# Optimization experiments

Measured on AMD Instinct MI355X. Metric: run time of the kernel, lower is better.

## Reference

```python
import jax, jax.numpy as jnp
import numpy as np

S, B, H = 4096, 32, 512

def setup_inputs() -> dict:
    key = jax.random.key(0)
    k1, k2, k3, k4, k5 = jax.random.split(key, 5)
    hidden = jax.random.normal(k1, (1, B, H), dtype=jnp.float32)
    encoder_outputs = jax.random.normal(k2, (S, B, H), dtype=jnp.float32)
    embedding = jax.random.normal(k3, (S, B, 3), dtype=jnp.float32)
    # learned params (xavier-ish scale)
    bigram_matrix = jax.random.normal(k4, (H, H), dtype=jnp.float32) * (1.0 / np.sqrt(H))
    affect_matrix = jax.random.normal(k5, (H, 3), dtype=jnp.float32) * 0.1
    return {"hidden": hidden, "encoder_outputs": encoder_outputs,
            "embedding": embedding, "bigram_matrix": bigram_matrix,
            "affect_matrix": affect_matrix}

def reference(hidden, encoder_outputs, embedding, bigram_matrix, affect_matrix):
    # hidden: [1,B,H] -> [B,H] (view(-1) over single layer)
    h = hidden[0]
    # bigram-modulated encoder states:
    #   i == 0: enc[0]
    #   i  > 0: (enc[i-1] @ W_bigram) * enc[i]
    modulated = jnp.einsum('sbh,hk->sbk', encoder_outputs[:-1], bigram_matrix) * encoder_outputs[1:]
    bigram_hidden = jnp.concatenate([encoder_outputs[:1], modulated], axis=0)  # [S,B,H]
    # dot-attention energy per (b, s)
    e_dot = jnp.einsum('sbh,bh->bs', bigram_hidden, h)  # [B,S]
    # affect term: (h @ affect_matrix) . embedding[s,b]
    e_aff = jnp.einsum('bk,sbk->bs', jnp.einsum('bh,hk->bk', h, affect_matrix), embedding)
    attn = jax.nn.softmax(e_dot + e_aff, axis=-1)  # softmax over seq dim
    return attn[:, None, :]  # [B,1,S]
```

## Files before the change

kernel.cpp:

```cpp
#include <hip/hip_runtime.h>
#include <cstdint>
#include <cstddef>

#define S_DIM 4096
#define B_DIM 32
#define H_DIM 512
#define M_DIM (S_DIM * B_DIM)

typedef unsigned short u16;
typedef unsigned int u32;
typedef float f32x4 __attribute__((ext_vector_type(4)));
typedef __bf16 bf16x8 __attribute__((ext_vector_type(8)));

__device__ __forceinline__ u16 f2bf(float v) {
    union { float f; u32 u; } a; a.f = v;
    u32 r = a.u + 0x7fffu + ((a.u >> 16) & 1u);
    return (u16)(r >> 16);
}
__device__ __forceinline__ float bf2f(u16 b) {
    union { float f; u32 u; } a; a.u = ((u32)b) << 16; return a.f;
}
__device__ __forceinline__ void split_bf(float v, u16& h, u16& l) {
    h = f2bf(v);
    l = f2bf(v - bf2f(h));
}

__device__ __forceinline__ void gl2lds16(const void* g, void* l) {
    __builtin_amdgcn_global_load_lds(
        (const __attribute__((address_space(1))) unsigned int*)g,
        (__attribute__((address_space(3))) unsigned int*)l,
        16, 0, 0);
}

__global__ void prep_w(const float* __restrict__ W,
                       u16* __restrict__ Wh, u16* __restrict__ Wl) {
    int i = blockIdx.x * 256 + threadIdx.x;
    float w = W[i];
    u16 h, l;
    split_bf(w, h, l);
    Wh[i] = h; Wl[i] = l;
}

__device__ __forceinline__ void split4_store(
    float4 e, float4 h, u16* dh, u16* dl)
{
    float vf[4] = { e.x * h.x, e.y * h.y, e.z * h.z, e.w * h.w };
    u32 rh[4], rl[4];
    #pragma unroll
    for (int i = 0; i < 4; ++i) {
        const u32 u = __float_as_uint(vf[i]);
        rh[i] = (u + 0x7fffu + ((u >> 16) & 1u)) & 0xffff0000u;
        const float lo_f = vf[i] - __uint_as_float(rh[i]);
        const u32 ul = __float_as_uint(lo_f);
        rl[i] = ul + 0x7fffu + ((ul >> 16) & 1u);
    }
    uint2 hw, lw;
    hw.x = rh[1] | (rh[0] >> 16);
    hw.y = rh[3] | (rh[2] >> 16);
    lw.x = (rl[1] & 0xffff0000u) | (rl[0] >> 16);
    lw.y = (rl[3] & 0xffff0000u) | (rl[2] >> 16);
    *(uint2*)dh = hw;
    *(uint2*)dl = lw;
}

__global__ __launch_bounds__(256, 2) void bigram_gemm_fused(
    const float* __restrict__ enc,
    const float* __restrict__ hid,
    const u16* __restrict__ Wh, const u16* __restrict__ Wl,
    float* __restrict__ Lp)
{
    __shared__ u16 sAh[2][128 * 32];
    __shared__ u16 sAl[2][128 * 32];
    __shared__ u16 sBh[2][128 * 32];
    __shared__ u16 sBl[2][128 * 32];
    __shared__ float rowsum[2][128];

    const int tid  = threadIdx.x;
    const int wave = tid >> 6;
    const int lane = tid & 63;
    const int wr   = wave >> 1;
    const int wc   = wave & 1;
    const int logical = (blockIdx.x & 7) * 512 + (blockIdx.x >> 3);
    const int jt   = logical & 3;
    const int mt   = logical >> 2;
    const int m0   = mt * 128;
    const int j0   = jt * 128;
    const int g    = lane >> 4;
    const int cl   = lane & 15;

    const int srow = wave * 32 + (lane >> 2);
    const int scol = (lane & 3) * 8;
    const size_t boff0 = (size_t)(j0 + srow) * H_DIM + scol;
    const size_t boff1 = boff0 + (size_t)16 * H_DIM;
    const u16* pBh0 = Wh + boff0; const u16* pBh1 = Wh + boff1;
    const u16* pBl0 = Wl + boff0; const u16* pBl1 = Wl + boff1;
    const int d0 = wave * 1024, d1 = d0 + 512;

    const int abrow = tid >> 3;
    const int akq   = tid & 7;
    const float* pe0 = enc + (size_t)(m0 +  0 + abrow) * H_DIM + akq * 4;
    const float* pe1 = enc + (size_t)(m0 + 32 + abrow) * H_DIM + akq * 4;
    const float* pe2 = enc + (size_t)(m0 + 64 + abrow) * H_DIM + akq * 4;
    const float* pe3 = enc + (size_t)(m0 + 96 + abrow) * H_DIM + akq * 4;
    const float* ph  = hid + (size_t)abrow * H_DIM + akq * 4;
    const int awoff = abrow * 32 + akq * 4;

    f32x4 acc[4][4];
    #pragma unroll
    for (int mf = 0; mf < 4; ++mf)
        #pragma unroll
        for (int nf = 0; nf < 4; ++nf)
            acc[mf][nf] = (f32x4){0.f, 0.f, 0.f, 0.f};

    {
        gl2lds16(pBh0, &sBh[0][d0]);
        gl2lds16(pBh1, &sBh[0][d1]);
        gl2lds16(pBl0, &sBl[0][d0]);
        gl2lds16(pBl1, &sBl[0][d1]);
        const float4 h0 = *(const float4*)ph;
        const float4 e0 = *(const float4*)pe0;
        const float4 e1 = *(const float4*)pe1;
        const float4 e2 = *(const float4*)pe2;
        const float4 e3 = *(const float4*)pe3;
        split4_store(e0, h0, &sAh[0][0 * 1024 + awoff], &sAl[0][0 * 1024 + awoff]);
        split4_store(e1, h0, &sAh[0][1 * 1024 + awoff], &sAl[0][1 * 1024 + awoff]);
        split4_store(e2, h0, &sAh[0][2 * 1024 + awoff], &sAl[0][2 * 1024 + awoff]);
        split4_store(e3, h0, &sAh[0][3 * 1024 + awoff], &sAl[0][3 * 1024 + awoff]);
    }
    __syncthreads();

    #pragma unroll 2
    for (int kt = 0; kt < 16; ++kt) {
        const int cur = kt & 1, nxt = cur ^ 1;
        const int ko = (kt + 1) * 32;

        float4 e0n, e1n, e2n, e3n, hn;
        if (kt < 15) {
            gl2lds16(pBh0 + ko, &sBh[nxt][d0]);
            gl2lds16(pBh1 + ko, &sBh[nxt][d1]);
            gl2lds16(pBl0 + ko, &sBl[nxt][d0]);
            gl2lds16(pBl1 + ko, &sBl[nxt][d1]);
            e0n = *(const float4*)(pe0 + ko);
            e1n = *(const float4*)(pe1 + ko);
            e2n = *(const float4*)(pe2 + ko);
            e3n = *(const float4*)(pe3 + ko);
            hn  = *(const float4*)(ph + ko);
        }

        bf16x8 ah[4], al[4], bh[4], bl[4];
        #pragma unroll
        for (int mf = 0; mf < 4; ++mf) {
            const int ar = wr * 64 + mf * 16 + cl;
            ah[mf] = *(const bf16x8*)(&sAh[cur][ar * 32 + g * 8]);
            al[mf] = *(const bf16x8*)(&sAl[cur][ar * 32 + g * 8]);
        }
        #pragma unroll
        for (int nf = 0; nf < 4; ++nf) {
            const int br = wc * 64 + nf * 16 + cl;
            bh[nf] = *(const bf16x8*)(&sBh[cur][br * 32 + g * 8]);
            bl[nf] = *(const bf16x8*)(&sBl[cur][br * 32 + g * 8]);
        }
        #pragma unroll
        for (int mf = 0; mf < 4; ++mf)
            #pragma unroll
            for (int nf = 0; nf < 4; ++nf) {
                acc[mf][nf] = __builtin_amdgcn_mfma_f32_16x16x32_bf16(ah[mf], bh[nf], acc[mf][nf], 0, 0, 0);
                acc[mf][nf] = __builtin_amdgcn_mfma_f32_16x16x32_bf16(ah[mf], bl[nf], acc[mf][nf], 0, 0, 0);
                acc[mf][nf] = __builtin_amdgcn_mfma_f32_16x16x32_bf16(al[mf], bh[nf], acc[mf][nf], 0, 0, 0);
            }

        if (kt < 15) {
            split4_store(e0n, hn, &sAh[nxt][0 * 1024 + awoff], &sAl[nxt][0 * 1024 + awoff]);
            split4_store(e1n, hn, &sAh[nxt][1 * 1024 + awoff], &sAl[nxt][1 * 1024 + awoff]);
            split4_store(e2n, hn, &sAh[nxt][2 * 1024 + awoff], &sAl[nxt][2 * 1024 + awoff]);
            split4_store(e3n, hn, &sAh[nxt][3 * 1024 + awoff], &sAl[nxt][3 * 1024 + awoff]);
        }
        __syncthreads();
    }

    #pragma unroll
    for (int mf = 0; mf < 4; ++mf) {
        float rs0 = 0.f, rs1 = 0.f, rs2 = 0.f, rs3 = 0.f;
        const int growb = m0 + wr * 64 + mf * 16 + g * 4;
        #pragma unroll
        for (int nf = 0; nf < 4; ++nf) {
            const int gcol = j0 + wc * 64 + nf * 16 + cl;
            float e0 = (growb + 0 >= B_DIM) ? enc[(size_t)(growb + 0 - B_DIM) * H_DIM + gcol] : 0.f;
            float e1 = (growb + 1 >= B_DIM) ? enc[(size_t)(growb + 1 - B_DIM) * H_DIM + gcol] : 0.f;
            float e2 = (growb + 2 >= B_DIM) ? enc[(size_t)(growb + 2 - B_DIM) * H_DIM + gcol] : 0.f;
            float e3 = (growb + 3 >= B_DIM) ? enc[(size_t)(growb + 3 - B_DIM) * H_DIM + gcol] : 0.f;
            rs0 += acc[mf][nf][0] * e0;
            rs1 += acc[mf][nf][1] * e1;
            rs2 += acc[mf][nf][2] * e2;
            rs3 += acc[mf][nf][3] * e3;
        }
        #pragma unroll
        for (int off = 1; off < 16; off <<= 1) {
            rs0 += __shfl_xor(rs0, off);
            rs1 += __shfl_xor(rs1, off);
            rs2 += __shfl_xor(rs2, off);
            rs3 += __shfl_xor(rs3, off);
        }
        if (cl == 0) {
            const int rb = wr * 64 + mf * 16 + g * 4;
            rowsum[wc][rb + 0] = rs0;
            rowsum[wc][rb + 1] = rs1;
            rowsum[wc][rb + 2] = rs2;
            rowsum[wc][rb + 3] = rs3;
        }
    }
    __syncthreads();
    if (tid < 128) {
        const int gm = m0 + tid;
        if (gm >= B_DIM) {
            Lp[(size_t)jt * M_DIM + (size_t)(gm & 31) * S_DIM + (gm >> 5)] =
                rowsum[0][tid] + rowsum[1][tid];
        }
    }
}

__global__ __launch_bounds__(256) void prep_aff(
    const float* __restrict__ enc,
    const float* __restrict__ hid,
    const float* __restrict__ aff,
    float* __restrict__ Aux)
{
    __shared__ float w[4][4];
    const int b    = blockIdx.x;
    const int tid  = threadIdx.x;
    const int wave = tid >> 6;
    const int lane = tid & 63;

    float p0 = 0.f, p1 = 0.f, p2 = 0.f, p3 = 0.f;
    #pragma unroll
    for (int it = 0; it < 2; ++it) {
        const int h = tid + it * 256;
        const float hv = hid[b * H_DIM + h];
        p0 += hv * aff[h * 3 + 0];
        p1 += hv * aff[h * 3 + 1];
        p2 += hv * aff[h * 3 + 2];
        p3 += hv * enc[(size_t)b * H_DIM + h];
    }
    #pragma unroll
    for (int off = 32; off > 0; off >>= 1) {
        p0 += __shfl_xor(p0, off);
        p1 += __shfl_xor(p1, off);
        p2 += __shfl_xor(p2, off);
        p3 += __shfl_xor(p3, off);
    }
    if (lane == 0) { w[wave][0] = p0; w[wave][1] = p1; w[wave][2] = p2; w[wave][3] = p3; }
    __syncthreads();
    if (tid < 4)
        Aux[b * 4 + tid] = w[0][tid] + w[1][tid] + w[2][tid] + w[3][tid];
}

__global__ __launch_bounds__(256) void sm_partial(
    const float* __restrict__ emb,
    const float* __restrict__ Lp,
    const float* __restrict__ Aux,
    float* __restrict__ Lg,
    float* __restrict__ Part)
{
    __shared__ float wm[4];
    __shared__ float wsum[4];
    const int b     = blockIdx.x >> 3;
    const int strip = blockIdx.x & 7;
    const int tid   = threadIdx.x;
    const int wave  = tid >> 6;
    const int lane  = tid & 63;

    const float ha0 = Aux[b * 4 + 0], ha1 = Aux[b * 4 + 1],
                ha2 = Aux[b * 4 + 2], s0dot = Aux[b * 4 + 3];

    float lgv[2];
    float mx = -3.4e38f;
    #pragma unroll
    for (int it = 0; it < 2; ++it) {
        const int s = strip * 512 + it * 256 + tid;
        const size_t base = (size_t)b * S_DIM + s;
        const float ed = (s == 0) ? s0dot
            : (Lp[base] + Lp[(size_t)M_DIM + base] + Lp[2 * (size_t)M_DIM + base] + Lp[3 * (size_t)M_DIM + base]);
        const float* e = emb + (size_t)(s * B_DIM + b) * 3;
        const float lg = ed + ha0 * e[0] + ha1 * e[1] + ha2 * e[2];
        Lg[(size_t)b * S_DIM + s] = lg;
        lgv[it] = lg;
        mx = fmaxf(mx, lg);
    }
    #pragma unroll
    for (int off = 32; off > 0; off >>= 1) mx = fmaxf(mx, __shfl_xor(mx, off));
    if (lane == 0) wm[wave] = mx;
    __syncthreads();
    mx = fmaxf(fmaxf(wm[0], wm[1]), fmaxf(wm[2], wm[3]));

    float sum = __expf(lgv[0] - mx) + __expf(lgv[1] - mx);
    #pragma unroll
    for (int off = 32; off > 0; off >>= 1) sum += __shfl_xor(sum, off);
    if (lane == 0) wsum[wave] = sum;
    __syncthreads();
    if (tid == 0) {
        Part[(size_t)(b * 8 + strip) * 2 + 0] = mx;
        Part[(size_t)(b * 8 + strip) * 2 + 1] = wsum[0] + wsum[1] + wsum[2] + wsum[3];
    }
}

__global__ __launch_bounds__(256) void sm_final(
    const float* __restrict__ Lg,
    const float* __restrict__ Part,
    float* __restrict__ out)
{
    const int b     = blockIdx.x >> 3;
    const int strip = blockIdx.x & 7;
    const int tid   = threadIdx.x;

    float M = -3.4e38f;
    #pragma unroll
    for (int i = 0; i < 8; ++i) M = fmaxf(M, Part[(size_t)(b * 8 + i) * 2]);
    float S = 0.f;
    #pragma unroll
    for (int i = 0; i < 8; ++i)
        S += Part[(size_t)(b * 8 + i) * 2 + 1] * __expf(Part[(size_t)(b * 8 + i) * 2] - M);
    const float inv = 1.0f / S;

    #pragma unroll
    for (int it = 0; it < 2; ++it) {
        const int s = strip * 512 + it * 256 + tid;
        out[(size_t)b * S_DIM + s] = __expf(Lg[(size_t)b * S_DIM + s] - M) * inv;
    }
}

extern "C" void kernel_launch(void* const* d_in, const int* in_sizes, int n_in,
                              void* d_out, int out_size, void* d_ws, size_t ws_size,
                              hipStream_t stream) {
    const float* hid = (const float*)d_in[0];
    const float* enc = (const float*)d_in[1];
    const float* emb = (const float*)d_in[2];
    const float* Wm  = (const float*)d_in[3];
    const float* aff = (const float*)d_in[4];
    float* out = (float*)d_out;

    char* ws = (char*)d_ws;
    u16*   Wh  = (u16*)ws;
    u16*   Wl  = (u16*)(ws + (512u << 10));
    float* Lp  = (float*)(ws + (1024u << 10));
    float* Aux = (float*)(ws + (3072u << 10));
    float* Lg  = (float*)(ws + (3072u << 10) + 1024);
    float* Part= (float*)(ws + (3072u << 10) + 1024 + (512u << 10));

    hipLaunchKernelGGL(prep_w, dim3(1024), dim3(256), 0, stream, Wm, Wh, Wl);
    hipLaunchKernelGGL(prep_aff, dim3(32), dim3(256), 0, stream, enc, hid, aff, Aux);
    hipLaunchKernelGGL(bigram_gemm_fused, dim3(4096), dim3(256), 0, stream,
                       enc, hid, Wh, Wl, Lp);
    hipLaunchKernelGGL(sm_partial, dim3(256), dim3(256), 0, stream,
                       emb, Lp, Aux, Lg, Part);
    hipLaunchKernelGGL(sm_final, dim3(256), dim3(256), 0, stream,
                       Lg, Part, out);
}
```

Before: 606.0 us.

## Single-buffer A tile in LDS and raise occupancy to three blocks per CU

The A-operand LDS tiles go from double to single buffering. A-fragments are loaded into registers first, then a barrier lets the next tile overwrite LDS while MFMAs run. Global loads of encoder rows are prefetched two k-steps ahead, and B fragments are now loaded per nf rather than all at once. Launch bounds move to three blocks per CU to raise occupancy. The cost is an extra barrier per iteration and tighter register pressure, which could cause spills.

```diff
diff --git a/kernel.cpp b/kernel.cpp
--- a/kernel.cpp
+++ b/kernel.cpp
@@ -63,14 +63,14 @@
     *(uint2*)dl = lw;
 }
 
-__global__ __launch_bounds__(256, 2) void bigram_gemm_fused(
+__global__ __launch_bounds__(256, 3) void bigram_gemm_fused(
     const float* __restrict__ enc,
     const float* __restrict__ hid,
     const u16* __restrict__ Wh, const u16* __restrict__ Wl,
     float* __restrict__ Lp)
 {
-    __shared__ u16 sAh[2][128 * 32];
-    __shared__ u16 sAl[2][128 * 32];
+    __shared__ u16 sAh[128 * 32];
+    __shared__ u16 sAl[128 * 32];
     __shared__ u16 sBh[2][128 * 32];
     __shared__ u16 sBl[2][128 * 32];
     __shared__ float rowsum[2][128];
@@ -112,71 +112,75 @@
         for (int nf = 0; nf < 4; ++nf)
             acc[mf][nf] = (f32x4){0.f, 0.f, 0.f, 0.f};
 
-    {
-        gl2lds16(pBh0, &sBh[0][d0]);
-        gl2lds16(pBh1, &sBh[0][d1]);
-        gl2lds16(pBl0, &sBl[0][d0]);
-        gl2lds16(pBl1, &sBl[0][d1]);
-        const float4 h0 = *(const float4*)ph;
-        const float4 e0 = *(const float4*)pe0;
-        const float4 e1 = *(const float4*)pe1;
-        const float4 e2 = *(const float4*)pe2;
-        const float4 e3 = *(const float4*)pe3;
-        split4_store(e0, h0, &sAh[0][0 * 1024 + awoff], &sAl[0][0 * 1024 + awoff]);
-        split4_store(e1, h0, &sAh[0][1 * 1024 + awoff], &sAl[0][1 * 1024 + awoff]);
-        split4_store(e2, h0, &sAh[0][2 * 1024 + awoff], &sAl[0][2 * 1024 + awoff]);
-        split4_store(e3, h0, &sAh[0][3 * 1024 + awoff], &sAl[0][3 * 1024 + awoff]);
-    }
-    __syncthreads();
-
-    #pragma unroll 2
-    for (int kt = 0; kt < 16; ++kt) {
-        const int cur = kt & 1, nxt = cur ^ 1;
-        const int ko = (kt + 1) * 32;
-
-        float4 e0n, e1n, e2n, e3n, hn;
-        if (kt < 15) {
-            gl2lds16(pBh0 + ko, &sBh[nxt][d0]);
-            gl2lds16(pBh1 + ko, &sBh[nxt][d1]);
-            gl2lds16(pBl0 + ko, &sBl[nxt][d0]);
-            gl2lds16(pBl1 + ko, &sBl[nxt][d1]);
-            e0n = *(const float4*)(pe0 + ko);
-            e1n = *(const float4*)(pe1 + ko);
-            e2n = *(const float4*)(pe2 + ko);
-            e3n = *(const float4*)(pe3 + ko);
-            hn  = *(const float4*)(ph + ko);
-        }
-
-        bf16x8 ah[4], al[4], bh[4], bl[4];
-        #pragma unroll
-        for (int mf = 0; mf < 4; ++mf) {
-            const int ar = wr * 64 + mf * 16 + cl;
-            ah[mf] = *(const bf16x8*)(&sAh[cur][ar * 32 + g * 8]);
-            al[mf] = *(const bf16x8*)(&sAl[cur][ar * 32 + g * 8]);
-        }
-        #pragma unroll
-        for (int nf = 0; nf < 4; ++nf) {
-            const int br = wc * 64 + nf * 16 + cl;
-            bh[nf] = *(const bf16x8*)(&sBh[cur][br * 32 + g * 8]);
-            bl[nf] = *(const bf16x8*)(&sBl[cur][br * 32 + g * 8]);
-        }
-        #pragma unroll
-        for (int mf = 0; mf < 4; ++mf)
-            #pragma unroll
-            for (int nf = 0; nf < 4; ++nf) {
-                acc[mf][nf] = __builtin_amdgcn_mfma_f32_16x16x32_bf16(ah[mf], bh[nf], acc[mf][nf], 0, 0, 0);
-                acc[mf][nf] = __builtin_amdgcn_mfma_f32_16x16x32_bf16(ah[mf], bl[nf], acc[mf][nf], 0, 0, 0);
-                acc[mf][nf] = __builtin_amdgcn_mfma_f32_16x16x32_bf16(al[mf], bh[nf], acc[mf][nf], 0, 0, 0);
-            }
-
-        if (kt < 15) {
-            split4_store(e0n, hn, &sAh[nxt][0 * 1024 + awoff], &sAl[nxt][0 * 1024 + awoff]);
-            split4_store(e1n, hn, &sAh[nxt][1 * 1024 + awoff], &sAl[nxt][1 * 1024 + awoff]);
-            split4_store(e2n, hn, &sAh[nxt][2 * 1024 + awoff], &sAl[nxt][2 * 1024 + awoff]);
-            split4_store(e3n, hn, &sAh[nxt][3 * 1024 + awoff], &sAl[nxt][3 * 1024 + awoff]);
-        }
-        __syncthreads();
-    }
+    float4 e0 = *(const float4*)pe0;
+    float4 e1 = *(const float4*)pe1;
+    float4 e2 = *(const float4*)pe2;
+    float4 e3 = *(const float4*)pe3;
+    float4 eh = *(const float4*)ph;
+    gl2lds16(pBh0, &sBh[0][d0]);
+    gl2lds16(pBh1, &sBh[0][d1]);
+    gl2lds16(pBl0, &sBl[0][d0]);
+    gl2lds16(pBl1, &sBl[0][d1]);
+    split4_store(e0, eh, sAh + 0 * 1024 + awoff, sAl + 0 * 1024 + awoff);
+    split4_store(e1, eh, sAh + 1 * 1024 + awoff, sAl + 1 * 1024 + awoff);
+    split4_store(e2, eh, sAh + 2 * 1024 + awoff, sAl + 2 * 1024 + awoff);
+    split4_store(e3, eh, sAh + 3 * 1024 + awoff, sAl + 3 * 1024 + awoff);
+    e0 = *(const float4*)(pe0 + 32);
+    e1 = *(const float4*)(pe1 + 32);
+    e2 = *(const float4*)(pe2 + 32);
+    e3 = *(const float4*)(pe3 + 32);
+    eh = *(const float4*)(ph + 32);
+    __syncthreads();
+
+#define GEMM_ITER(KT, CUR)                                                     \
+  {                                                                            \
+    bf16x8 ah[4], al[4];                                                       \
+    _Pragma("unroll")                                                          \
+    for (int mf = 0; mf < 4; ++mf) {                                           \
+      const int ar = wr * 64 + mf * 16 + cl;                                   \
+      ah[mf] = *(const bf16x8*)(sAh + ar * 32 + g * 8);                        \
+      al[mf] = *(const bf16x8*)(sAl + ar * 32 + g * 8);                        \
+    }                                                                          \
+    __syncthreads();  \
+    if ((KT) < 15) {                                                           \
+      const int ko = ((KT) + 1) * 32;                                          \
+      gl2lds16(pBh0 + ko, &sBh[(CUR) ^ 1][d0]);                                \
+      gl2lds16(pBh1 + ko, &sBh[(CUR) ^ 1][d1]);                                \
+      gl2lds16(pBl0 + ko, &sBl[(CUR) ^ 1][d0]);                                \
+      gl2lds16(pBl1 + ko, &sBl[(CUR) ^ 1][d1]);                                \
+      split4_store(e0, eh, sAh + 0 * 1024 + awoff, sAl + 0 * 1024 + awoff);    \
+      split4_store(e1, eh, sAh + 1 * 1024 + awoff, sAl + 1 * 1024 + awoff);    \
+      split4_store(e2, eh, sAh + 2 * 1024 + awoff, sAl + 2 * 1024 + awoff);    \
+      split4_store(e3, eh, sAh + 3 * 1024 + awoff, sAl + 3 * 1024 + awoff);    \
+    }                                                                          \
+    if ((KT) < 14) {                                                           \
+      const int ko2 = ((KT) + 2) * 32;                                         \
+      e0 = *(const float4*)(pe0 + ko2);                                        \
+      e1 = *(const float4*)(pe1 + ko2);                                        \
+      e2 = *(const float4*)(pe2 + ko2);                                        \
+      e3 = *(const float4*)(pe3 + ko2);                                        \
+      eh = *(const float4*)(ph + ko2);                                         \
+    }                                                                          \
+    _Pragma("unroll")                                                          \
+    for (int nf = 0; nf < 4; ++nf) {                                           \
+      const int br = wc * 64 + nf * 16 + cl;                                   \
+      const bf16x8 bh = *(const bf16x8*)(&sBh[(CUR)][br * 32 + g * 8]);        \
+      const bf16x8 bl = *(const bf16x8*)(&sBl[(CUR)][br * 32 + g * 8]);        \
+      _Pragma("unroll")                                                        \
+      for (int mf = 0; mf < 4; ++mf) {                                         \
+        acc[mf][nf] = __builtin_amdgcn_mfma_f32_16x16x32_bf16(ah[mf], bh, acc[mf][nf], 0, 0, 0); \
+        acc[mf][nf] = __builtin_amdgcn_mfma_f32_16x16x32_bf16(ah[mf], bl, acc[mf][nf], 0, 0, 0); \
+        acc[mf][nf] = __builtin_amdgcn_mfma_f32_16x16x32_bf16(al[mf], bh, acc[mf][nf], 0, 0, 0); \
+      }                                                                        \
+    }                                                                          \
+    __syncthreads();    \
+  }
+
+    for (int kt = 0; kt < 16; kt += 2) {
+        GEMM_ITER(kt, 0);
+        GEMM_ITER(kt + 1, 1);
+    }
+#undef GEMM_ITER
 
     #pragma unroll
     for (int mf = 0; mf < 4; ++mf) {
@@ -185,14 +189,14 @@
         #pragma unroll
         for (int nf = 0; nf < 4; ++nf) {
             const int gcol = j0 + wc * 64 + nf * 16 + cl;
-            float e0 = (growb + 0 >= B_DIM) ? enc[(size_t)(growb + 0 - B_DIM) * H_DIM + gcol] : 0.f;
-            float e1 = (growb + 1 >= B_DIM) ? enc[(size_t)(growb + 1 - B_DIM) * H_DIM + gcol] : 0.f;
-            float e2 = (growb + 2 >= B_DIM) ? enc[(size_t)(growb + 2 - B_DIM) * H_DIM + gcol] : 0.f;
-            float e3 = (growb + 3 >= B_DIM) ? enc[(size_t)(growb + 3 - B_DIM) * H_DIM + gcol] : 0.f;
-            rs0 += acc[mf][nf][0] * e0;
-            rs1 += acc[mf][nf][1] * e1;
-            rs2 += acc[mf][nf][2] * e2;
-            rs3 += acc[mf][nf][3] * e3;
+            float ee0 = (growb + 0 >= B_DIM) ? enc[(size_t)(growb + 0 - B_DIM) * H_DIM + gcol] : 0.f;
+            float ee1 = (growb + 1 >= B_DIM) ? enc[(size_t)(growb + 1 - B_DIM) * H_DIM + gcol] : 0.f;
+            float ee2 = (growb + 2 >= B_DIM) ? enc[(size_t)(growb + 2 - B_DIM) * H_DIM + gcol] : 0.f;
+            float ee3 = (growb + 3 >= B_DIM) ? enc[(size_t)(growb + 3 - B_DIM) * H_DIM + gcol] : 0.f;
+            rs0 += acc[mf][nf][0] * ee0;
+            rs1 += acc[mf][nf][1] * ee1;
+            rs2 += acc[mf][nf][2] * ee2;
+            rs3 += acc[mf][nf][3] * ee3;
         }
         #pragma unroll
         for (int off = 1; off < 16; off <<= 1) {
```

After: 558.5 us. 1.09x faster.
